# Optimization experiments

Measured on AMD Instinct MI355X. Metric: run time of the kernel, lower is better.

## Reference

```python
import jax, jax.numpy as jnp
import numpy as np

B, S, H = 2, 2048, 2048
NH, HD = 16, 128
I = 8192
EPS = float(np.finfo(np.float32).eps)  # torch RMSNorm default eps=None -> dtype eps


def rmsnorm(x, w):
    var = jnp.mean(jnp.square(x), axis=-1, keepdims=True)
    return x * jax.lax.rsqrt(var + EPS) * w


def setup_inputs() -> dict:
    key = jax.random.key(0)
    ks = jax.random.split(key, 8)
    s = 0.02
    return {
        "hidden_states": jax.random.normal(ks[0], (B, S, H), jnp.float32),
        "Wq": jax.random.normal(ks[1], (H, H), jnp.float32) * s,
        "Wk": jax.random.normal(ks[2], (H, H), jnp.float32) * s,
        "Wv": jax.random.normal(ks[3], (H, H), jnp.float32) * s,
        "Wo": jax.random.normal(ks[4], (H, H), jnp.float32) * s,
        "Wg": jax.random.normal(ks[5], (I, H), jnp.float32) * s,
        "Wu": jax.random.normal(ks[6], (I, H), jnp.float32) * s,
        "Wd": jax.random.normal(ks[7], (H, I), jnp.float32) * s,
        "g_in": jnp.ones((H,), jnp.float32),
        "g_post": jnp.ones((H,), jnp.float32),
    }


def reference(hidden_states, Wq, Wk, Wv, Wo, Wg, Wu, Wd, g_in, g_post):
    residual = hidden_states
    x = rmsnorm(hidden_states, g_in)
    # projections: nn.Linear does x @ W.T
    q = (x @ Wq.T).reshape(B, S, NH, HD).transpose(0, 2, 1, 3)  # [B,NH,S,HD]
    k = (x @ Wk.T).reshape(B, S, NH, HD).transpose(0, 2, 1, 3)
    v = (x @ Wv.T).reshape(B, S, NH, HD).transpose(0, 2, 1, 3)
    scores = jnp.einsum("bhqd,bhkd->bhqk", q, k) / jnp.sqrt(jnp.float32(HD))
    attn = jax.nn.softmax(scores, axis=-1)
    out = jnp.einsum("bhqk,bhkd->bhqd", attn, v)
    out = out.transpose(0, 2, 1, 3).reshape(B, S, H)
    hidden_states = residual + out @ Wo.T
    residual = hidden_states
    x = rmsnorm(hidden_states, g_post)
    mlp = (jax.nn.silu(x @ Wg.T) * (x @ Wu.T)) @ Wd.T
    return residual + mlp
```

## Files before the change

### kernel.cpp

```cpp
#include <hip/hip_runtime.h>

using u16 = unsigned short;
using u32 = unsigned int;

typedef __attribute__((ext_vector_type(8))) __bf16 bf16x8;
typedef __attribute__((ext_vector_type(4))) float f32x4;

__device__ __forceinline__ u16 f2bf(float f) {
  __bf16 h = (__bf16)f;
  return __builtin_bit_cast(u16, h);
}
__device__ __forceinline__ u32 pk2(float a, float b) {
  return (u32)f2bf(a) | ((u32)f2bf(b) << 16);
}
__device__ __forceinline__ float bf2f(u16 h) {
  return __uint_as_float(((u32)h) << 16);
}
__device__ __forceinline__ void gload16(const u16* g, u16* l) {
  __builtin_amdgcn_global_load_lds((const __attribute__((address_space(1))) void*)g,
                                   (__attribute__((address_space(3))) void*)l, 16, 0, 0);
}
__device__ __forceinline__ f32x4 mfma_bf16(bf16x8 a, bf16x8 b, f32x4 c) {
  return __builtin_amdgcn_mfma_f32_16x16x32_bf16(a, b, c, 0, 0, 0);
}

__global__ __launch_bounds__(256) void cvt_bf16(const float* __restrict__ in,
                                                u16* __restrict__ out, int n8) {
  int i = blockIdx.x * 256 + threadIdx.x;
  int stride = gridDim.x * 256;
  for (; i < n8; i += stride) {
    float4 a = ((const float4*)in)[(size_t)i * 2];
    float4 b = ((const float4*)in)[(size_t)i * 2 + 1];
    ((uint4*)out)[i] = make_uint4(pk2(a.x, a.y), pk2(a.z, a.w), pk2(b.x, b.y), pk2(b.z, b.w));
  }
}

__global__ __launch_bounds__(256) void rmsnorm_bf16(const float* __restrict__ x,
                                                    const float* __restrict__ g,
                                                    u16* __restrict__ o) {
  const int row = blockIdx.x;
  const int tid = threadIdx.x;
  const float4* xr = (const float4*)(x + (size_t)row * 2048);
  float4 a = xr[tid * 2], b = xr[tid * 2 + 1];
  float s = a.x * a.x + a.y * a.y + a.z * a.z + a.w * a.w +
            b.x * b.x + b.y * b.y + b.z * b.z + b.w * b.w;
#pragma unroll
  for (int off = 1; off < 64; off <<= 1) s += __shfl_xor(s, off);
  __shared__ float red[4];
  if ((tid & 63) == 0) red[tid >> 6] = s;
  __syncthreads();
  s = red[0] + red[1] + red[2] + red[3];
  const float r = rsqrtf(s * (1.0f / 2048.0f) + 1.1920929e-07f);
  const float4* gr = (const float4*)g;
  float4 ga = gr[tid * 2], gb = gr[tid * 2 + 1];
  ((uint4*)(o + (size_t)row * 2048))[tid] =
      make_uint4(pk2(a.x * r * ga.x, a.y * r * ga.y), pk2(a.z * r * ga.z, a.w * r * ga.w),
                 pk2(b.x * r * gb.x, b.y * r * gb.y), pk2(b.z * r * gb.z, b.w * r * gb.w));
}

__global__ __launch_bounds__(512, 2) void gemmGU(const u16* __restrict__ A,
                                                 const u16* __restrict__ Bg,
                                                 const u16* __restrict__ Bu,
                                                 u16* __restrict__ Out,
                                                 int M, int N, int K) {
  alignas(16) __shared__ u16 lds[2 * 32768];
  const int tid = threadIdx.x;
  const int w = tid >> 6, lane = tid & 63;
  const int lo = lane & 15, hi = lane >> 4;
  const int nbm = M >> 8, nbx = N >> 7;
  const int RM = nbm >> 1, RN = nbx >> 2;
  const int xcd = blockIdx.x & 7, bidx = blockIdx.x >> 3;
  const int bm = ((xcd >> 2) * RM + bidx / RN) << 8;
  const int bn = ((xcd & 3) * RN + bidx % RN) << 7;
  const int wm = w >> 1, wn = w & 1;

  const int rw = (hi ^ ((lo >> 1) & 3)) * 8;
  const int arow0 = wm * 64 + lo, brow0 = wn * 64 + lo;

  const int srow = tid >> 2;
  const int scol = ((tid & 3) ^ ((tid >> 3) & 3)) * 8;
  const u16* Ab = A + (size_t)(bm + srow) * K + scol;
  const u16* Bgb = Bg + (size_t)(bn + srow) * K + scol;
  const u16* Bub = Bu + (size_t)(bn + srow) * K + scol;

  f32x4 gacc[4][4] = {}, uacc[4][4] = {};
  bf16x8 af[4], bf[4];

#define AOFF(par, kh) ((par)*32768 + (kh)*8192)
#define BGOFF(par, kh) ((par)*32768 + 16384 + (kh)*4096)
#define BUOFF(par, kh) ((par)*32768 + 24576 + (kh)*4096)
#define STG_A(par, kh, kt)                                                  \
  {                                                                         \
    gload16(Ab + (kt) + (kh)*32, &lds[AOFF(par, kh) + tid * 8]);            \
    gload16(Ab + (size_t)128 * K + (kt) + (kh)*32,                          \
            &lds[AOFF(par, kh) + 4096 + tid * 8]);                          \
  }
#define STG_B(par, kh, kt)                                                  \
  {                                                                         \
    gload16(Bgb + (kt) + (kh)*32, &lds[BGOFF(par, kh) + tid * 8]);          \
    gload16(Bub + (kt) + (kh)*32, &lds[BUOFF(par, kh) + tid * 8]);          \
  }
#define PHASE_OPEN()                                   \
  __builtin_amdgcn_s_barrier();                        \
  asm volatile("s_waitcnt lgkmcnt(0)" ::: "memory");   \
  __builtin_amdgcn_sched_barrier(0);
#define MFMA16(ACC)                                                         \
  __builtin_amdgcn_s_setprio(1);                                            \
  _Pragma("unroll") for (int m_ = 0; m_ < 4; ++m_)                          \
      _Pragma("unroll") for (int n_ = 0; n_ < 4; ++n_)                      \
          ACC[m_][n_] = mfma_bf16(af[m_], bf[n_], ACC[m_][n_]);             \
  __builtin_amdgcn_s_setprio(0);

  STG_A(0, 0, 0); STG_B(0, 0, 0); STG_A(0, 1, 0); STG_B(0, 1, 0);
  asm volatile("s_waitcnt vmcnt(0)" ::: "memory");
  __builtin_amdgcn_s_barrier();

  const int NT = K >> 6;
  for (int t = 0; t < NT; ++t) {
    const int par = t & 1, np = par ^ 1;
    const int ktn = (t + 1) << 6;
    const bool pre = (t + 1 < NT);

#pragma unroll
    for (int n = 0; n < 4; ++n)
      bf[n] = *(const bf16x8*)(&lds[BGOFF(par, 0)] + (brow0 + n * 16) * 32 + rw);
#pragma unroll
    for (int m = 0; m < 4; ++m)
      af[m] = *(const bf16x8*)(&lds[AOFF(par, 0)] + (arow0 + m * 16) * 32 + rw);
    if (pre) STG_A(np, 0, ktn);
    PHASE_OPEN();
    MFMA16(gacc);
    __builtin_amdgcn_s_barrier();

#pragma unroll
    for (int n = 0; n < 4; ++n)
      bf[n] = *(const bf16x8*)(&lds[BUOFF(par, 0)] + (brow0 + n * 16) * 32 + rw);
    if (pre) STG_B(np, 0, ktn);
    PHASE_OPEN();
    MFMA16(uacc);
    if (pre) { asm volatile("s_waitcnt vmcnt(4)" ::: "memory"); }
    else     { asm volatile("s_waitcnt vmcnt(0)" ::: "memory"); }
    __builtin_amdgcn_s_barrier();

#pragma unroll
    for (int n = 0; n < 4; ++n)
      bf[n] = *(const bf16x8*)(&lds[BGOFF(par, 1)] + (brow0 + n * 16) * 32 + rw);
#pragma unroll
    for (int m = 0; m < 4; ++m)
      af[m] = *(const bf16x8*)(&lds[AOFF(par, 1)] + (arow0 + m * 16) * 32 + rw);
    if (pre) STG_A(np, 1, ktn);
    PHASE_OPEN();
    MFMA16(gacc);
    __builtin_amdgcn_s_barrier();

#pragma unroll
    for (int n = 0; n < 4; ++n)
      bf[n] = *(const bf16x8*)(&lds[BUOFF(par, 1)] + (brow0 + n * 16) * 32 + rw);
    if (pre) STG_B(np, 1, ktn);
    PHASE_OPEN();
    MFMA16(uacc);
    if (pre) { asm volatile("s_waitcnt vmcnt(4)" ::: "memory"); }
    __builtin_amdgcn_s_barrier();
  }
#undef AOFF
#undef BGOFF
#undef BUOFF
#undef STG_A
#undef STG_B
#undef PHASE_OPEN
#undef MFMA16

#pragma unroll
  for (int m = 0; m < 4; ++m) {
    const int gr = bm + wm * 64 + m * 16 + hi * 4;
#pragma unroll
    for (int n = 0; n < 4; ++n) {
      const int gc = bn + wn * 64 + n * 16 + lo;
#pragma unroll
      for (int r = 0; r < 4; ++r) {
        float g = gacc[m][n][r];
        float s = g / (1.f + __expf(-g));
        Out[(size_t)(gr + r) * N + gc] = f2bf(s * uacc[m][n][r]);
      }
    }
  }
}

template <int EPI>
__global__ __launch_bounds__(512, 1) void gemm3b(const u16* __restrict__ A,
                                                 const u16* __restrict__ B,
                                                 u16* Cb, float* Cf,
                                                 const float* __restrict__ Res,
                                                 int M, int N, int K, int lda) {
  constexpr int BUF = 24576;
  alignas(16) __shared__ u16 lds[3 * BUF];
  const int tid = threadIdx.x;
  const int w = tid >> 6, lane = tid & 63;
  const int lo = lane & 15, hi = lane >> 4;

  const int nbm = M >> 8, nbx = N >> 7;
  const int RM = nbm >> 1, RN = nbx >> 2;
  const int xcd = blockIdx.x & 7, idx = blockIdx.x >> 3;
  const int bm = ((xcd >> 2) * RM + idx / RN) << 8;
  const int bn = ((xcd & 3) * RN + idx % RN) << 7;

  const int wm = w >> 1, wn = w & 1;
  const int scol = ((tid & 7) ^ ((tid >> 3) & 7)) * 8;
  const u16* Ag = A + (size_t)(bm + (tid >> 3)) * lda + scol;
  const u16* Bg = B + (size_t)(bn + (tid >> 3)) * K + scol;

  f32x4 acc[4][4] = {};

#define STG(b, kt)                                                                    \
  {                                                                                   \
    _Pragma("unroll") for (int c = 0; c < 4; ++c)                                     \
        gload16(Ag + (size_t)(c * 64) * lda + (kt), &lds[(b)*BUF + c * 4096 + tid * 8]); \
    _Pragma("unroll") for (int c = 0; c < 2; ++c)                                     \
        gload16(Bg + (size_t)(c * 64) * K + (kt), &lds[(b)*BUF + 16384 + c * 4096 + tid * 8]); \
  }

  const int NT = K >> 6;
  STG(0, 0);
  STG(1, 64);

  int cur = 0;
  for (int T = 0; T < NT; ++T) {
    if (T + 1 < NT) {
      asm volatile("s_waitcnt vmcnt(6)" ::: "memory");
    } else {
      asm volatile("s_waitcnt vmcnt(0)" ::: "memory");
    }
    __builtin_amdgcn_s_barrier();
    __builtin_amdgcn_sched_barrier(0);

    const u16* LA = &lds[cur * BUF];
    const u16* LB = LA + 16384;
    bf16x8 af[4][2], bf[4][2];
#pragma unroll
    for (int ks = 0; ks < 2; ++ks) {
#pragma unroll
      for (int m = 0; m < 4; ++m)
        af[m][ks] = *(const bf16x8*)(LA + (wm * 64 + m * 16 + lo) * 64 +
                                     ((ks * 4 + hi) ^ (lo & 7)) * 8);
#pragma unroll
      for (int n = 0; n < 4; ++n)
        bf[n][ks] = *(const bf16x8*)(LB + (wn * 64 + n * 16 + lo) * 64 +
                                     ((ks * 4 + hi) ^ (lo & 7)) * 8);
    }
    if (T + 2 < NT) {
      const int nb = (cur + 2) % 3;
      STG(nb, (T + 2) << 6);
    }
    __builtin_amdgcn_s_setprio(1);
#pragma unroll
    for (int ks = 0; ks < 2; ++ks)
#pragma unroll
      for (int m = 0; m < 4; ++m)
#pragma unroll
        for (int n = 0; n < 4; ++n) acc[m][n] = mfma_bf16(af[m][ks], bf[n][ks], acc[m][n]);
    __builtin_amdgcn_s_setprio(0);
    cur = (cur + 1) % 3;
  }
#undef STG

#pragma unroll
  for (int m = 0; m < 4; ++m) {
    const int gr = bm + wm * 64 + m * 16 + hi * 4;
#pragma unroll
    for (int n = 0; n < 4; ++n) {
      const int gc = bn + wn * 64 + n * 16 + lo;
#pragma unroll
      for (int r = 0; r < 4; ++r) {
        const size_t idx2 = (size_t)(gr + r) * N + gc;
        if constexpr (EPI == 1) {
          Cf[idx2] = Res[idx2] + acc[m][n][r];
        } else if constexpr (EPI == 2) {
          float g = bf2f(Cb[idx2]);
          float s = g / (1.f + __expf(-g));
          Cb[idx2] = f2bf(s * acc[m][n][r]);
        } else {
          Cb[idx2] = f2bf(acc[m][n][r]);
        }
      }
    }
  }
}

template <int EPI>
__global__ __launch_bounds__(256) void gemm_bt(const u16* __restrict__ A,
                                               const float* __restrict__ B,
                                               u16* Cb, float* Cf, const float* Res,
                                               int M, int N, int K) {
  alignas(16) __shared__ u16 As[128 * 32];
  alignas(16) __shared__ u16 Bs[128 * 32];
  const int tid = threadIdx.x;
  const int w = tid >> 6, lane = tid & 63;
  const int lo = lane & 15, hi = lane >> 4;
  const int bm = blockIdx.y * 128, bn = blockIdx.x * 128;
  const int wr = (w >> 1) * 64, wc = (w & 1) * 64;
  f32x4 acc[4][4] = {};
  const int r0 = tid >> 2, kc0 = (tid & 3) * 8;
  const u16* a0 = A + (size_t)(bm + r0) * K + kc0;
  const u16* a1 = A + (size_t)(bm + 64 + r0) * K + kc0;
  const float* b0 = B + (size_t)(bn + r0) * K + kc0;
  const float* b1 = B + (size_t)(bn + 64 + r0) * K + kc0;
  u16* asd0 = &As[(size_t)tid * 8];
  u16* asd1 = &As[(size_t)(tid + 256) * 8];
  u16* bsd0 = &Bs[(size_t)tid * 8];
  u16* bsd1 = &Bs[(size_t)(tid + 256) * 8];
  for (int kt = 0; kt < K; kt += 32) {
    gload16(a0 + kt, asd0);
    gload16(a1 + kt, asd1);
    float4 x0 = *(const float4*)(b0 + kt);
    float4 x1 = *(const float4*)(b0 + kt + 4);
    float4 y0 = *(const float4*)(b1 + kt);
    float4 y1 = *(const float4*)(b1 + kt + 4);
    *(uint4*)bsd0 = make_uint4(pk2(x0.x, x0.y), pk2(x0.z, x0.w), pk2(x1.x, x1.y), pk2(x1.z, x1.w));
    *(uint4*)bsd1 = make_uint4(pk2(y0.x, y0.y), pk2(y0.z, y0.w), pk2(y1.x, y1.y), pk2(y1.z, y1.w));
    __syncthreads();
    bf16x8 af[4], bfr[4];
#pragma unroll
    for (int i = 0; i < 4; ++i) {
      af[i] = *(const bf16x8*)(&As[(wr + i * 16 + lo) * 32 + hi * 8]);
      bfr[i] = *(const bf16x8*)(&Bs[(wc + i * 16 + lo) * 32 + hi * 8]);
    }
#pragma unroll
    for (int i = 0; i < 4; ++i)
#pragma unroll
      for (int j = 0; j < 4; ++j) acc[i][j] = mfma_bf16(af[i], bfr[j], acc[i][j]);
    __syncthreads();
  }
#pragma unroll
  for (int i = 0; i < 4; ++i) {
    const int gr = bm + wr + i * 16 + hi * 4;
#pragma unroll
    for (int j = 0; j < 4; ++j) {
      const int gc = bn + wc + j * 16 + lo;
#pragma unroll
      for (int r = 0; r < 4; ++r) {
        const size_t idx = (size_t)(gr + r) * N + gc;
        if constexpr (EPI == 1) {
          Cf[idx] = Res[idx] + acc[i][j][r];
        } else if constexpr (EPI == 2) {
          float g = bf2f(Cb[idx]);
          float s = g / (1.f + __expf(-g));
          Cb[idx] = f2bf(s * acc[i][j][r]);
        } else {
          Cb[idx] = f2bf(acc[i][j][r]);
        }
      }
    }
  }
}

__global__ __launch_bounds__(256) void transpose_v(const u16* __restrict__ v,
                                                   u16* __restrict__ vt, int ldv) {
  __shared__ u16 t[32][33];
  const int bh = blockIdx.z, b = bh >> 4, h = bh & 15;
  const int s0 = blockIdx.x * 32, d0 = blockIdx.y * 32;
  const int tx = threadIdx.x, ty = threadIdx.y;
#pragma unroll
  for (int i = 0; i < 4; ++i)
    t[ty + i * 8][tx] = v[(size_t)(b * 2048 + s0 + ty + i * 8) * ldv + h * 128 + d0 + tx];
  __syncthreads();
#pragma unroll
  for (int i = 0; i < 4; ++i)
    vt[(size_t)(bh * 128 + d0 + ty + i * 8) * 2048 + s0 + tx] = t[tx][ty + i * 8];
}

__global__ __launch_bounds__(512) void attn_fwd3(const u16* __restrict__ q,
                                                 const u16* __restrict__ k,
                                                 const u16* __restrict__ vt,
                                                 u16* o, int ldq) {
  constexpr int S = 2048;
  alignas(16) __shared__ u16 Ks[2][64 * 128];
  alignas(16) __shared__ u16 Vs[2][128 * 64];
  alignas(16) __shared__ u16 plds[8][16 * 68];
  const int bh = blockIdx.y, b = bh >> 4, h = bh & 15;
  const int tid = threadIdx.x, w = tid >> 6, lane = tid & 63;
  const int lo = lane & 15, hi = lane >> 4;
  const int qr = blockIdx.x * 128 + w * 16;
  u16* pl = &plds[w][0];

  bf16x8 qf[4];
  const u16* qb = q + (size_t)(b * S + qr + lo) * ldq + h * 128 + hi * 8;
#pragma unroll
  for (int ks = 0; ks < 4; ++ks) qf[ks] = *(const bf16x8*)(qb + ks * 32);

  f32x4 oacc[8] = {};
  f32x4 lp = {0.f, 0.f, 0.f, 0.f};

  const u16* kb = k + (size_t)(b * S) * ldq + h * 128;
  const u16* vb = vt + (size_t)bh * 128 * S;

  const int kcs = ((tid & 15) ^ ((tid >> 4) & 7)) * 8;
  const int vcs = ((tid & 7) ^ ((tid >> 3) & 7)) * 8;
  const u16* kgs = kb + (size_t)(tid >> 4) * ldq + kcs;
  const u16* vgs = vb + (size_t)(tid >> 3) * S + vcs;

  int cur = 0;
#pragma unroll
  for (int c = 0; c < 2; ++c) gload16(kgs + (size_t)(c * 32) * ldq, &Ks[0][c * 4096 + tid * 8]);
#pragma unroll
  for (int c = 0; c < 2; ++c) gload16(vgs + (size_t)(c * 64) * S, &Vs[0][c * 4096 + tid * 8]);
  __syncthreads();

  const int swq = (lo & 7) << 4;
  constexpr float SCL = 0.12752956f;

  for (int kv = 0; kv < S; kv += 64) {
    if (kv + 64 < S) {
      const int nb = cur ^ 1;
#pragma unroll
      for (int c = 0; c < 2; ++c)
        gload16(kgs + (size_t)(kv + 64 + c * 32) * ldq, &Ks[nb][c * 4096 + tid * 8]);
#pragma unroll
      for (int c = 0; c < 2; ++c)
        gload16(vgs + (size_t)(c * 64) * S + kv + 64, &Vs[nb][c * 4096 + tid * 8]);
    }
    const u16* Kc = &Ks[cur][0];
    const u16* Vc = &Vs[cur][0];

    f32x4 sacc[4] = {};
    __builtin_amdgcn_s_setprio(1);
#pragma unroll
    for (int ks = 0; ks < 4; ++ks)
#pragma unroll
      for (int n = 0; n < 4; ++n) {
        bf16x8 kf = *(const bf16x8*)(Kc + (n * 16 + lo) * 128 + (((ks * 64 + hi * 16) ^ swq) >> 1));
        sacc[n] = mfma_bf16(qf[ks], kf, sacc[n]);
      }
    __builtin_amdgcn_s_setprio(0);

    f32x4 p[4];
#pragma unroll
    for (int n = 0; n < 4; ++n)
#pragma unroll
      for (int r = 0; r < 4; ++r) p[n][r] = exp2f(sacc[n][r] * SCL);
#pragma unroll
    for (int r = 0; r < 4; ++r)
      lp[r] += (p[0][r] + p[1][r]) + (p[2][r] + p[3][r]);

#pragma unroll
    for (int n = 0; n < 4; ++n)
#pragma unroll
      for (int r = 0; r < 4; ++r)
        pl[(hi * 4 + r) * 68 + n * 16 + lo] = f2bf(p[n][r]);
    asm volatile("s_waitcnt lgkmcnt(0)" ::: "memory");
    bf16x8 pf0 = *(const bf16x8*)(pl + lo * 68 + hi * 8);
    bf16x8 pf1 = *(const bf16x8*)(pl + lo * 68 + 32 + hi * 8);

    __builtin_amdgcn_s_setprio(1);
#pragma unroll
    for (int f = 0; f < 8; ++f) {
      const int row = f * 16 + lo;
      bf16x8 vf0 = *(const bf16x8*)(Vc + row * 64 + (((hi * 16) ^ swq) >> 1));
      bf16x8 vf1 = *(const bf16x8*)(Vc + row * 64 + (((64 + hi * 16) ^ swq) >> 1));
      oacc[f] = mfma_bf16(pf0, vf0, oacc[f]);
      oacc[f] = mfma_bf16(pf1, vf1, oacc[f]);
    }
    __builtin_amdgcn_s_setprio(0);

    __syncthreads();
    cur ^= 1;
  }

  float l[4];
#pragma unroll
  for (int r = 0; r < 4; ++r) l[r] = lp[r];
#pragma unroll
  for (int off = 1; off < 16; off <<= 1)
#pragma unroll
    for (int r = 0; r < 4; ++r) l[r] += __shfl_xor(l[r], off);

  u16* ob = o + (size_t)(b * S + qr) * ldq + h * 128;
#pragma unroll
  for (int f = 0; f < 8; ++f)
#pragma unroll
    for (int r = 0; r < 4; ++r)
      ob[(size_t)(hi * 4 + r) * ldq + f * 16 + lo] = f2bf(oacc[f][r] / l[r]);
}

extern "C" void kernel_launch(void* const* d_in, const int* in_sizes, int n_in,
                              void* d_out, int out_size, void* d_ws, size_t ws_size,
                              hipStream_t stream) {
  constexpr int B = 2, S = 2048, H = 2048, NH = 16, I = 8192;
  constexpr int M = B * S;

  const float* hs = (const float*)d_in[0];
  const float* Wq = (const float*)d_in[1];
  const float* Wk = (const float*)d_in[2];
  const float* Wv = (const float*)d_in[3];
  const float* Wo = (const float*)d_in[4];
  const float* Wg = (const float*)d_in[5];
  const float* Wu = (const float*)d_in[6];
  const float* Wd = (const float*)d_in[7];
  const float* g_in = (const float*)d_in[8];
  const float* g_post = (const float*)d_in[9];
  float* out = (float*)d_out;

  constexpr size_t SZ_HH = (size_t)H * H * 2;
  constexpr size_t SZ_IH = (size_t)I * H * 2;
  constexpr size_t SZ_MH = (size_t)M * H * 2;
  constexpr size_t NEED_BASE = SZ_MH + 3 * SZ_MH + SZ_MH + SZ_IH;
  constexpr size_t NEED_FUSED = NEED_BASE + SZ_IH;

  if (ws_size >= NEED_BASE) {
    char* p = (char*)d_ws;
    u16* x_b = (u16*)p;    p += SZ_MH;
    u16* qkv_b = (u16*)p;  p += 3 * SZ_MH;
    u16* vt_b = (u16*)p;   p += SZ_MH;
    u16* wsc = (u16*)p;    p += SZ_IH;
    u16* gate_b = qkv_b;
    const bool fused = ws_size >= NEED_FUSED;
    u16* wu_b = fused ? (u16*)p : nullptr;

    rmsnorm_bf16<<<M, 256, 0, stream>>>(hs, g_in, x_b);

    cvt_bf16<<<1024, 256, 0, stream>>>(Wq, wsc, H * H / 8);
    cvt_bf16<<<1024, 256, 0, stream>>>(Wk, wsc + (size_t)H * H, H * H / 8);
    cvt_bf16<<<1024, 256, 0, stream>>>(Wv, wsc + (size_t)2 * H * H, H * H / 8);
    gemm3b<0><<<(M / 256) * (3 * H / 128), 512, 0, stream>>>(
        x_b, wsc, qkv_b, nullptr, nullptr, M, 3 * H, H, H);

    transpose_v<<<dim3(S / 32, 128 / 32, B * NH), dim3(32, 8), 0, stream>>>(
        qkv_b + 2 * H, vt_b, 3 * H);
    attn_fwd3<<<dim3(S / 128, B * NH), 512, 0, stream>>>(qkv_b, qkv_b + H, vt_b, qkv_b, 3 * H);

    cvt_bf16<<<1024, 256, 0, stream>>>(Wo, wsc, H * H / 8);
    gemm3b<1><<<(M / 256) * (H / 128), 512, 0, stream>>>(
        qkv_b, wsc, nullptr, out, hs, M, H, H, 3 * H);

    rmsnorm_bf16<<<M, 256, 0, stream>>>(out, g_post, x_b);

    if (fused) {
      cvt_bf16<<<1024, 256, 0, stream>>>(Wg, wsc, I * H / 8);
      cvt_bf16<<<1024, 256, 0, stream>>>(Wu, wu_b, I * H / 8);
      gemmGU<<<(M / 256) * (I / 128), 512, 0, stream>>>(x_b, wsc, wu_b, gate_b, M, I, H);
    } else {
      cvt_bf16<<<1024, 256, 0, stream>>>(Wg, wsc, I * H / 8);
      gemm3b<0><<<(M / 256) * (I / 128), 512, 0, stream>>>(
          x_b, wsc, gate_b, nullptr, nullptr, M, I, H, H);
      cvt_bf16<<<1024, 256, 0, stream>>>(Wu, wsc, I * H / 8);
      gemm3b<2><<<(M / 256) * (I / 128), 512, 0, stream>>>(
          x_b, wsc, gate_b, nullptr, nullptr, M, I, H, H);
    }
    cvt_bf16<<<1024, 256, 0, stream>>>(Wd, wsc, I * H / 8);
    gemm3b<1><<<(M / 256) * (H / 128), 512, 0, stream>>>(
        gate_b, wsc, nullptr, out, out, M, H, I, I);
    return;
  }

  constexpr int MC = 2048;
  char* p = (char*)d_ws;
  u16* x_b = (u16*)p;   p += SZ_MH;
  u16* q_b = (u16*)p;   p += SZ_MH;
  u16* k_b = (u16*)p;   p += SZ_MH;
  u16* v_b = (u16*)p;   p += SZ_MH;
  u16* vt_b = (u16*)p;  p += SZ_MH;
  u16* g_mlp = k_b;

  rmsnorm_bf16<<<M, 256, 0, stream>>>(hs, g_in, x_b);
  const dim3 gHH(H / 128, M / 128);
  gemm_bt<0><<<gHH, 256, 0, stream>>>(x_b, Wq, q_b, nullptr, nullptr, M, H, H);
  gemm_bt<0><<<gHH, 256, 0, stream>>>(x_b, Wk, k_b, nullptr, nullptr, M, H, H);
  gemm_bt<0><<<gHH, 256, 0, stream>>>(x_b, Wv, v_b, nullptr, nullptr, M, H, H);
  transpose_v<<<dim3(S / 32, 128 / 32, B * NH), dim3(32, 8), 0, stream>>>(v_b, vt_b, H);
  attn_fwd3<<<dim3(S / 128, B * NH), 512, 0, stream>>>(q_b, k_b, vt_b, q_b, H);
  gemm_bt<1><<<gHH, 256, 0, stream>>>(q_b, Wo, nullptr, out, hs, M, H, H);
  rmsnorm_bf16<<<M, 256, 0, stream>>>(out, g_post, x_b);
  const dim3 gIH(I / 128, MC / 128), gHI(H / 128, MC / 128);
  for (int mc = 0; mc < M / MC; ++mc) {
    const u16* xc = x_b + (size_t)mc * MC * H;
    float* oc = out + (size_t)mc * MC * H;
    gemm_bt<0><<<gIH, 256, 0, stream>>>(xc, Wg, g_mlp, nullptr, nullptr, MC, I, H);
    gemm_bt<2><<<gIH, 256, 0, stream>>>(xc, Wu, g_mlp, nullptr, nullptr, MC, I, H);
    gemm_bt<1><<<gHI, 256, 0, stream>>>(g_mlp, Wd, nullptr, oc, oc, MC, H, I);
  }
}
```

Before: 779.1 us.

## Batch all weight conversions into one launch and trim barriers in gate/up GEMM

Adds a single cvt_all kernel that converts all seven fp32 weight matrices to bf16 in one launch, used when the workspace is large enough to hold every converted weight. The previous path issued several separate conversion launches, some interleaved between GEMMs. The gemmGU main loop now has one barrier per phase instead of two, with the vmcnt waits moved ahead of the barrier that opens the next phase. This cuts launch overhead and synchronization stalls, but needs a larger workspace and front-loads all conversion traffic before the first GEMM.

```diff
diff --git a/kernel.cpp b/kernel.cpp
--- a/kernel.cpp
+++ b/kernel.cpp
@@ -32,6 +32,27 @@
     float4 a = ((const float4*)in)[(size_t)i * 2];
     float4 b = ((const float4*)in)[(size_t)i * 2 + 1];
     ((uint4*)out)[i] = make_uint4(pk2(a.x, a.y), pk2(a.z, a.w), pk2(b.x, b.y), pk2(b.z, b.w));
+  }
+}
+
+struct CvtJobs {
+  const float* in[7];
+  u16* out[7];
+  int n8[7];
+};
+__global__ __launch_bounds__(256) void cvt_all(CvtJobs c) {
+  const int stride = gridDim.x * 256;
+  const int base = blockIdx.x * 256 + threadIdx.x;
+#pragma unroll
+  for (int j = 0; j < 7; ++j) {
+    const float* in = c.in[j];
+    u16* out = c.out[j];
+    const int n8 = c.n8[j];
+    for (int i = base; i < n8; i += stride) {
+      float4 a = ((const float4*)in)[(size_t)i * 2];
+      float4 b = ((const float4*)in)[(size_t)i * 2 + 1];
+      ((uint4*)out)[i] = make_uint4(pk2(a.x, a.y), pk2(a.z, a.w), pk2(b.x, b.y), pk2(b.z, b.w));
+    }
   }
 }
 
@@ -100,7 +121,7 @@
     gload16(Bgb + (kt) + (kh)*32, &lds[BGOFF(par, kh) + tid * 8]);          \
     gload16(Bub + (kt) + (kh)*32, &lds[BUOFF(par, kh) + tid * 8]);          \
   }
-#define PHASE_OPEN()                                   \
+#define PHASE_SYNC()                                   \
   __builtin_amdgcn_s_barrier();                        \
   asm volatile("s_waitcnt lgkmcnt(0)" ::: "memory");   \
   __builtin_amdgcn_sched_barrier(0);
@@ -128,19 +149,17 @@
     for (int m = 0; m < 4; ++m)
       af[m] = *(const bf16x8*)(&lds[AOFF(par, 0)] + (arow0 + m * 16) * 32 + rw);
     if (pre) STG_A(np, 0, ktn);
-    PHASE_OPEN();
+    PHASE_SYNC();
     MFMA16(gacc);
-    __builtin_amdgcn_s_barrier();
 
 #pragma unroll
     for (int n = 0; n < 4; ++n)
       bf[n] = *(const bf16x8*)(&lds[BUOFF(par, 0)] + (brow0 + n * 16) * 32 + rw);
     if (pre) STG_B(np, 0, ktn);
-    PHASE_OPEN();
-    MFMA16(uacc);
     if (pre) { asm volatile("s_waitcnt vmcnt(4)" ::: "memory"); }
     else     { asm volatile("s_waitcnt vmcnt(0)" ::: "memory"); }
-    __builtin_amdgcn_s_barrier();
+    PHASE_SYNC();
+    MFMA16(uacc);
 
 #pragma unroll
     for (int n = 0; n < 4; ++n)
@@ -149,25 +168,23 @@
     for (int m = 0; m < 4; ++m)
       af[m] = *(const bf16x8*)(&lds[AOFF(par, 1)] + (arow0 + m * 16) * 32 + rw);
     if (pre) STG_A(np, 1, ktn);
-    PHASE_OPEN();
+    PHASE_SYNC();
     MFMA16(gacc);
-    __builtin_amdgcn_s_barrier();
 
 #pragma unroll
     for (int n = 0; n < 4; ++n)
       bf[n] = *(const bf16x8*)(&lds[BUOFF(par, 1)] + (brow0 + n * 16) * 32 + rw);
     if (pre) STG_B(np, 1, ktn);
-    PHASE_OPEN();
+    if (pre) { asm volatile("s_waitcnt vmcnt(4)" ::: "memory"); }
+    PHASE_SYNC();
     MFMA16(uacc);
-    if (pre) { asm volatile("s_waitcnt vmcnt(4)" ::: "memory"); }
-    __builtin_amdgcn_s_barrier();
   }
 #undef AOFF
 #undef BGOFF
 #undef BUOFF
 #undef STG_A
 #undef STG_B
-#undef PHASE_OPEN
+#undef PHASE_SYNC
 #undef MFMA16
 
 #pragma unroll
@@ -502,8 +519,52 @@
   constexpr size_t SZ_HH = (size_t)H * H * 2;
   constexpr size_t SZ_IH = (size_t)I * H * 2;
   constexpr size_t SZ_MH = (size_t)M * H * 2;
+  constexpr size_t NEED_ALL = 5 * SZ_MH + 3 * SZ_HH + SZ_HH + 3 * SZ_IH;
+  constexpr size_t NEED_FUSED = SZ_MH + 3 * SZ_MH + SZ_MH + 2 * SZ_IH;
   constexpr size_t NEED_BASE = SZ_MH + 3 * SZ_MH + SZ_MH + SZ_IH;
-  constexpr size_t NEED_FUSED = NEED_BASE + SZ_IH;
+
+  if (ws_size >= NEED_ALL) {
+    char* p = (char*)d_ws;
+    u16* x_b = (u16*)p;    p += SZ_MH;
+    u16* qkv_b = (u16*)p;  p += 3 * SZ_MH;
+    u16* vt_b = (u16*)p;   p += SZ_MH;
+    u16* wqkv = (u16*)p;   p += 3 * SZ_HH;
+    u16* wo_b = (u16*)p;   p += SZ_HH;
+    u16* wg_b = (u16*)p;   p += SZ_IH;
+    u16* wu_b = (u16*)p;   p += SZ_IH;
+    u16* wd_b = (u16*)p;   p += SZ_IH;
+    u16* gate_b = qkv_b;
+
+    rmsnorm_bf16<<<M, 256, 0, stream>>>(hs, g_in, x_b);
+
+    CvtJobs cj;
+    cj.in[0] = Wq;  cj.out[0] = wqkv;                     cj.n8[0] = H * H / 8;
+    cj.in[1] = Wk;  cj.out[1] = wqkv + (size_t)H * H;     cj.n8[1] = H * H / 8;
+    cj.in[2] = Wv;  cj.out[2] = wqkv + (size_t)2 * H * H; cj.n8[2] = H * H / 8;
+    cj.in[3] = Wo;  cj.out[3] = wo_b;                     cj.n8[3] = H * H / 8;
+    cj.in[4] = Wg;  cj.out[4] = wg_b;                     cj.n8[4] = I * H / 8;
+    cj.in[5] = Wu;  cj.out[5] = wu_b;                     cj.n8[5] = I * H / 8;
+    cj.in[6] = Wd;  cj.out[6] = wd_b;                     cj.n8[6] = I * H / 8;
+    cvt_all<<<2048, 256, 0, stream>>>(cj);
+
+    gemm3b<0><<<(M / 256) * (3 * H / 128), 512, 0, stream>>>(
+        x_b, wqkv, qkv_b, nullptr, nullptr, M, 3 * H, H, H);
+
+    transpose_v<<<dim3(S / 32, 128 / 32, B * NH), dim3(32, 8), 0, stream>>>(
+        qkv_b + 2 * H, vt_b, 3 * H);
+    attn_fwd3<<<dim3(S / 128, B * NH), 512, 0, stream>>>(qkv_b, qkv_b + H, vt_b, qkv_b, 3 * H);
+
+    gemm3b<1><<<(M / 256) * (H / 128), 512, 0, stream>>>(
+        qkv_b, wo_b, nullptr, out, hs, M, H, H, 3 * H);
+
+    rmsnorm_bf16<<<M, 256, 0, stream>>>(out, g_post, x_b);
+
+    gemmGU<<<(M / 256) * (I / 128), 512, 0, stream>>>(x_b, wg_b, wu_b, gate_b, M, I, H);
+
+    gemm3b<1><<<(M / 256) * (H / 128), 512, 0, stream>>>(
+        gate_b, wd_b, nullptr, out, out, M, H, I, I);
+    return;
+  }
 
   if (ws_size >= NEED_BASE) {
     char* p = (char*)d_ws;
```

Result: no change. 782.7 us (+0.5%).
